# Performance work log

Hardware: AMD Instinct MI355X
Metric: run time of the kernel (lower is better)

The kernel has to match this reference:

```python
import jax, jax.numpy as jnp
import numpy as np
from jax import lax

H = 128  # hidden_size


def lstm_last_h(x, w_ih, w_hh, b_ih, b_hh):
    """PyTorch-style single-layer LSTM; returns final hidden state.
    x: (B, T, D). Gate order i, f, g, o. w_ih: (4H, D), w_hh: (4H, H)."""
    B = x.shape[0]
    Hh = w_hh.shape[1]
    x_proj = jnp.einsum('btd,gd->btg', x, w_ih) + b_ih + b_hh  # (B, T, 4H)

    def step(carry, xt):
        h, c = carry
        gates = xt + h @ w_hh.T
        i, f, g, o = jnp.split(gates, 4, axis=-1)
        i = jax.nn.sigmoid(i)
        f = jax.nn.sigmoid(f)
        g = jnp.tanh(g)
        o = jax.nn.sigmoid(o)
        c = f * c + i * g
        h = o * jnp.tanh(c)
        return (h, c), None

    init = (jnp.zeros((B, Hh), x.dtype), jnp.zeros((B, Hh), x.dtype))
    (h, _), _ = lax.scan(step, init, jnp.swapaxes(x_proj, 0, 1))
    return h  # (B, H)


def setup_inputs() -> dict:
    key = jax.random.key(0)
    ks = jax.random.split(key, 12)
    s = 0.05
    return {
        'x_players': jax.random.normal(ks[0], (64, 22, 128, 2), jnp.float32),
        'x_ball': jax.random.normal(ks[1], (64, 128, 2), jnp.float32),
        'p_w_ih': jax.random.normal(ks[2], (4 * H, 2), jnp.float32) * s,
        'p_w_hh': jax.random.normal(ks[3], (4 * H, H), jnp.float32) * s,
        'p_b_ih': jax.random.normal(ks[4], (4 * H,), jnp.float32) * s,
        'p_b_hh': jax.random.normal(ks[5], (4 * H,), jnp.float32) * s,
        'b_w_ih': jax.random.normal(ks[6], (4 * H, 2), jnp.float32) * s,
        'b_w_hh': jax.random.normal(ks[7], (4 * H, H), jnp.float32) * s,
        'b_b_ih': jax.random.normal(ks[8], (4 * H,), jnp.float32) * s,
        'b_b_hh': jax.random.normal(ks[9], (4 * H,), jnp.float32) * s,
        'fc_w': jax.random.normal(ks[10], (40, 2 * H), jnp.float32) * s,
        'fc_b': jax.random.normal(ks[11], (40,), jnp.float32) * s,
    }


def reference(x_players, x_ball, p_w_ih, p_w_hh, p_b_ih, p_b_hh,
              b_w_ih, b_w_hh, b_b_ih, b_b_hh, fc_w, fc_b):
    B, P, T, D = x_players.shape
    ball_h = lstm_last_h(x_ball, b_w_ih, b_w_hh, b_b_ih, b_b_hh)  # (B, H)
    # Shared player LSTM: fold players into batch (replaces per-player loop).
    ph = lstm_last_h(x_players.reshape(B * P, T, D),
                     p_w_ih, p_w_hh, p_b_ih, p_b_hh).reshape(B, P, H)
    ball_rep = jnp.broadcast_to(ball_h[:, None, :], (B, P, H))
    combined = jnp.concatenate([ph, ball_rep], axis=-1)  # (B, P, 2H)
    out = combined @ fc_w.T + fc_b  # (B, P, 40)
    return out.reshape(B, P, 20, 2)
```

## Files before the change

### kernel.cpp

```cpp
#include <hip/hip_runtime.h>


#define HDIM 128
#define TSTEPS 128
#define NPLAYER 1408
#define NSEQ 1472
#define NB 8
#define NBLK (NSEQ / NB)
#define NPBLK (NPLAYER / NB)
#define KT 5
#define BSTR 168
#define XSTR 258
#define HSTR 132

typedef _Float16 f16x8 __attribute__((ext_vector_type(8)));
typedef _Float16 f16x2 __attribute__((ext_vector_type(2)));
typedef float    f32x4 __attribute__((ext_vector_type(4)));
typedef float    f32x2 __attribute__((ext_vector_type(2)));

#define LOG2E 1.44269504f

__device__ __forceinline__ f32x2 exp2v(f32x2 a) {
    return (f32x2){__builtin_amdgcn_exp2f(a[0]), __builtin_amdgcn_exp2f(a[1])};
}
__device__ __forceinline__ f32x2 rcpv(f32x2 a) {
    return (f32x2){__builtin_amdgcn_rcpf(a[0]), __builtin_amdgcn_rcpf(a[1])};
}
__device__ __forceinline__ float dpp_sel8(float keep, float src) {
    return __int_as_float(__builtin_amdgcn_update_dpp(
        __float_as_int(keep), __float_as_int(src), 0x128 ,
        0xF, 0xC, false));
}

__global__ void __launch_bounds__(512)
__attribute__((amdgpu_waves_per_eu(2, 2)))
lstm_fc_kernel(const float* __restrict__ x_players, const float* __restrict__ x_ball,
               const float* __restrict__ p_w_ih, const float* __restrict__ p_w_hh,
               const float* __restrict__ p_b_ih, const float* __restrict__ p_b_hh,
               const float* __restrict__ b_w_ih, const float* __restrict__ b_w_hh,
               const float* __restrict__ b_b_ih, const float* __restrict__ b_b_hh,
               const float* __restrict__ fc_w, const float* __restrict__ fc_b,
               float* __restrict__ out)
{
    const int tid  = threadIdx.x;
    const int blk  = blockIdx.x;
    const int w    = tid >> 6;
    const int lane = tid & 63;
    const int nn   = lane & 15;
    const int q    = lane >> 4;

    const bool ball = (blk >= NPBLK);
    const float* w_ih = ball ? b_w_ih : p_w_ih;
    const float* w_hh = ball ? b_w_hh : p_w_hh;
    const float* bih  = ball ? b_b_ih : p_b_ih;
    const float* bhh  = ball ? b_b_hh : p_b_hh;
    const float* xg   = ball ? (x_ball    + (size_t)(blk - NPBLK) * NB * TSTEPS * 2)
                             : (x_players + (size_t)blk * NB * TSTEPS * 2);

    __shared__ __align__(16) _Float16 b_sh[2][NB * BSTR];
    __shared__ __align__(16) float x_sh[NB * XSTR];
    __shared__ __align__(16) float hbuf[NB * HSTR];
    __shared__ float vout[NB * 40];

    for (int i = tid; i < NB * 256; i += 512)
        x_sh[(i >> 8) * XSTR + (i & 255)] = xg[i];
    for (int i = tid; i < 2 * NB * BSTR / 2; i += 512)
        ((int*)b_sh)[i] = 0;

    f16x8 afr[4][KT];
    #pragma unroll
    for (int mi = 0; mi < 4; ++mi) {
        const int r = mi * HDIM + w * 16 + nn;
        const float* wr = w_hh + (size_t)r * HDIM;
        #pragma unroll
        for (int kt = 0; kt < 4; ++kt) {
            const float* p = wr + kt * 32 + q * 8;
            f16x8 a8;
            #pragma unroll
            for (int j = 0; j < 8; ++j) a8[j] = (_Float16)p[j];
            afr[mi][kt] = a8;
        }
        f16x8 a8 = {};
        if (q == 0) {
            a8[0] = (_Float16)w_ih[2 * r];
            a8[1] = (_Float16)w_ih[2 * r + 1];
            a8[2] = (_Float16)(bih[r] + bhh[r]);
        }
        afr[mi][4] = a8;
    }

    const int colh   = nn & 7;
    const int rowoff = (nn < 8) ? 0 : 2;
    const int hrow   = w * 16 + 4 * q + rowoff;
    f32x2 c = (f32x2){0.f, 0.f};
    f32x2 h = (f32x2){0.f, 0.f};

    f32x4 zero4 = (f32x4){0.f, 0.f, 0.f, 0.f};
    asm volatile("" : "+v"(zero4));

    __syncthreads();
    if (tid < NB) {
        _Float16* br0 = &b_sh[0][tid * BSTR];
        br0[128] = (_Float16)x_sh[tid * XSTR];
        br0[129] = (_Float16)x_sh[tid * XSTR + 1];
        br0[130] = (_Float16)1.0f;
        b_sh[1][tid * BSTR + 130] = (_Float16)1.0f;
    }
    __syncthreads();

    f16x8 bfr[KT] = {};

    auto substep = [&](int s, const _Float16* bc, _Float16* bn, bool last) {
        if (nn < 8) {
            #pragma unroll
            for (int kt = 0; kt < KT; ++kt)
                bfr[kt] = *(const f16x8*)(bc + nn * BSTR + kt * 32 + q * 8);
        }

        f32x4 acc[4];
        #pragma unroll
        for (int mi = 0; mi < 4; ++mi)
            acc[mi] = __builtin_amdgcn_mfma_f32_16x16x32_f16(afr[mi][4], bfr[4], zero4, 0, 0, 0);
        #pragma unroll
        for (int kt = 0; kt < 4; ++kt)
            #pragma unroll
            for (int mi = 0; mi < 4; ++mi)
                acc[mi] = __builtin_amdgcn_mfma_f32_16x16x32_f16(afr[mi][kt], bfr[kt], acc[mi], 0, 0, 0);

        if (!last && tid < NB) {
            const float x0 = x_sh[tid * XSTR + 2 * (s + 1)];
            const float x1 = x_sh[tid * XSTR + 2 * (s + 1) + 1];
            *(f16x2*)&bn[tid * BSTR + 128] = (f16x2){(_Float16)x0, (_Float16)x1};
        }

        f32x2 u[4];
        #pragma unroll
        for (int mi = 0; mi < 4; ++mi) {
            u[mi][0] = dpp_sel8(acc[mi][0], acc[mi][2]);
            u[mi][1] = dpp_sel8(acc[mi][1], acc[mi][3]);
        }

        const f32x2 ei = exp2v(u[0] * -LOG2E);
        const f32x2 ef = exp2v(u[1] * -LOG2E);
        const f32x2 eg = exp2v(u[2] * (2.0f * LOG2E));
        const f32x2 eo = exp2v(u[3] * -LOG2E);
        const f32x2 ig = (eg - 1.0f) * rcpv((ei + 1.0f) * (eg + 1.0f));
        const f32x2 ff = rcpv(ef + 1.0f);
        c = __builtin_elementwise_fma(ff, c, ig);
        c = __builtin_elementwise_min(__builtin_elementwise_max(c, (f32x2){-15.f, -15.f}),
                                      (f32x2){15.f, 15.f});
        const f32x2 ec = exp2v(c * (2.0f * LOG2E));
        h = (ec - 1.0f) * rcpv((eo + 1.0f) * (ec + 1.0f));

        if (!last) {
            *(f16x2*)&bn[colh * BSTR + hrow] = (f16x2){(_Float16)h[0], (_Float16)h[1]};
            __syncthreads();
        }
    };

    _Float16* b0 = &b_sh[0][0];
    _Float16* b1 = &b_sh[1][0];
    #pragma unroll 1
    for (int it = 0; it < TSTEPS / 2 - 1; ++it) {
        substep(2 * it,     b0, b1, false);
        substep(2 * it + 1, b1, b0, false);
        asm volatile("" : "+a"(afr[0][0]), "+a"(afr[0][1]), "+a"(afr[0][2]), "+a"(afr[0][3]), "+a"(afr[0][4]));
        asm volatile("" : "+a"(afr[1][0]), "+a"(afr[1][1]), "+a"(afr[1][2]), "+a"(afr[1][3]), "+a"(afr[1][4]));
        asm volatile("" : "+a"(afr[2][0]), "+a"(afr[2][1]), "+a"(afr[2][2]), "+a"(afr[2][3]), "+a"(afr[2][4]));
        asm volatile("" : "+a"(afr[3][0]), "+a"(afr[3][1]), "+a"(afr[3][2]), "+a"(afr[3][3]), "+a"(afr[3][4]));
        asm volatile("" : "+v"(zero4));
    }
    substep(126, b0, b1, false);
    substep(127, b1, b0, true);

    hbuf[colh * HSTR + hrow]     = h[0];
    hbuf[colh * HSTR + hrow + 1] = h[1];
    __syncthreads();

    if (!ball) {
        for (int o = tid; o < NB * 40; o += 512) {
            const int j = o / 40, row = o - j * 40;
            const float* wr = fc_w + (size_t)row * 2 * HDIM;
            const float* hp = &hbuf[j * HSTR];
            float a0 = fc_b[row], a1 = 0.f, a2 = 0.f, a3 = 0.f;
            #pragma unroll
            for (int k = 0; k < HDIM; k += 4) {
                float4 wv = *(const float4*)(wr + k);
                float4 hv = *(const float4*)(hp + k);
                a0 = __builtin_fmaf(wv.x, hv.x, a0);
                a1 = __builtin_fmaf(wv.y, hv.y, a1);
                a2 = __builtin_fmaf(wv.z, hv.z, a2);
                a3 = __builtin_fmaf(wv.w, hv.w, a3);
            }
            atomicAdd(&out[(size_t)(NB * blk + j) * 40 + row], (a0 + a1) + (a2 + a3));
        }
    } else {
        for (int o = tid; o < NB * 40; o += 512) {
            const int cc = o / 40, row = o - cc * 40;
            const float* wr = fc_w + (size_t)row * 2 * HDIM + HDIM;
            const float* hp = &hbuf[cc * HSTR];
            float a0 = 0.f, a1 = 0.f, a2 = 0.f, a3 = 0.f;
            #pragma unroll
            for (int k = 0; k < HDIM; k += 4) {
                float4 wv = *(const float4*)(wr + k);
                float4 hv = *(const float4*)(hp + k);
                a0 = __builtin_fmaf(wv.x, hv.x, a0);
                a1 = __builtin_fmaf(wv.y, hv.y, a1);
                a2 = __builtin_fmaf(wv.z, hv.z, a2);
                a3 = __builtin_fmaf(wv.w, hv.w, a3);
            }
            vout[cc * 40 + row] = (a0 + a1) + (a2 + a3);
        }
        __syncthreads();
        const int base_batch = (blk - NPBLK) * NB;
        for (int o = tid; o < NB * 22 * 40; o += 512) {
            const int cc = o / 880, rem = o - cc * 880;
            const int p = rem / 40, row = rem - p * 40;
            atomicAdd(&out[(size_t)((base_batch + cc) * 22 + p) * 40 + row],
                      vout[cc * 40 + row]);
        }
    }
}

extern "C" void kernel_launch(void* const* d_in, const int* in_sizes, int n_in,
                              void* d_out, int out_size, void* d_ws, size_t ws_size,
                              hipStream_t stream) {
    const float* x_players = (const float*)d_in[0];
    const float* x_ball    = (const float*)d_in[1];
    const float* p_w_ih    = (const float*)d_in[2];
    const float* p_w_hh    = (const float*)d_in[3];
    const float* p_b_ih    = (const float*)d_in[4];
    const float* p_b_hh    = (const float*)d_in[5];
    const float* b_w_ih    = (const float*)d_in[6];
    const float* b_w_hh    = (const float*)d_in[7];
    const float* b_b_ih    = (const float*)d_in[8];
    const float* b_b_hh    = (const float*)d_in[9];
    const float* fc_w      = (const float*)d_in[10];
    const float* fc_b      = (const float*)d_in[11];

    hipMemsetAsync(d_out, 0, (size_t)out_size * sizeof(float), stream);

    lstm_fc_kernel<<<dim3(NBLK), dim3(512), 0, stream>>>(
        x_players, x_ball, p_w_ih, p_w_hh, p_b_ih, p_b_hh,
        b_w_ih, b_w_hh, b_b_ih, b_b_hh, fc_w, fc_b, (float*)d_out);
}
```

Before: 181.8 us.

## Split gate work across 16 waves with flag-based producer/consumer exchange

Doubles the block to 1024 threads. Each wave now holds two gate tiles instead of four: waves 0-7 compute the i and g gates, and waves 8-15 compute the f and o gates. The f/o waves write their sigmoids to shared memory and raise a per-wave flag, while the i/g waves spin on that flag and then finish the cell and hidden-state update. This halves the serial MFMA and transcendental chain per wave and trades it for extra shared-memory traffic, spin-waits, a wider barrier and halved occupancy per block.

```diff
diff --git a/kernel.cpp b/kernel.cpp
--- a/kernel.cpp
+++ b/kernel.cpp
@@ -12,6 +12,7 @@
 #define BSTR 168
 #define XSTR 258
 #define HSTR 132
+#define ESTR 10
 
 typedef _Float16 f16x8 __attribute__((ext_vector_type(8)));
 typedef _Float16 f16x2 __attribute__((ext_vector_type(2)));
@@ -28,12 +29,11 @@
 }
 __device__ __forceinline__ float dpp_sel8(float keep, float src) {
     return __int_as_float(__builtin_amdgcn_update_dpp(
-        __float_as_int(keep), __float_as_int(src), 0x128 ,
-        0xF, 0xC, false));
-}
-
-__global__ void __launch_bounds__(512)
-__attribute__((amdgpu_waves_per_eu(2, 2)))
+        __float_as_int(keep), __float_as_int(src), 0x128 , 0xF, 0xC, false));
+}
+
+__global__ void __launch_bounds__(1024)
+__attribute__((amdgpu_waves_per_eu(4, 4)))
 lstm_fc_kernel(const float* __restrict__ x_players, const float* __restrict__ x_ball,
                const float* __restrict__ p_w_ih, const float* __restrict__ p_w_hh,
                const float* __restrict__ p_b_ih, const float* __restrict__ p_b_hh,
@@ -48,6 +48,9 @@
     const int lane = tid & 63;
     const int nn   = lane & 15;
     const int q    = lane >> 4;
+    const int b3   = (nn >> 3) & 1;
+    const int w8   = w & 7;
+    const bool heavy = (w < 8);
 
     const bool ball = (blk >= NPBLK);
     const float* w_ih = ball ? b_w_ih : p_w_ih;
@@ -59,18 +62,22 @@
 
     __shared__ __align__(16) _Float16 b_sh[2][NB * BSTR];
     __shared__ __align__(16) float x_sh[NB * XSTR];
+    __shared__ float exF[HDIM * ESTR];
+    __shared__ float exO[HDIM * ESTR];
+    __shared__ int   flags[8];
     __shared__ __align__(16) float hbuf[NB * HSTR];
     __shared__ float vout[NB * 40];
 
-    for (int i = tid; i < NB * 256; i += 512)
+    for (int i = tid; i < NB * 256; i += 1024)
         x_sh[(i >> 8) * XSTR + (i & 255)] = xg[i];
-    for (int i = tid; i < 2 * NB * BSTR / 2; i += 512)
+    for (int i = tid; i < 2 * NB * BSTR / 2; i += 1024)
         ((int*)b_sh)[i] = 0;
-
-    f16x8 afr[4][KT];
+    if (tid < 8) flags[tid] = 0;
+
+    f16x8 afr[2][KT];
     #pragma unroll
-    for (int mi = 0; mi < 4; ++mi) {
-        const int r = mi * HDIM + w * 16 + nn;
+    for (int ti = 0; ti < 2; ++ti) {
+        const int r = 16 * (w + 16 * ti) + nn;
         const float* wr = w_hh + (size_t)r * HDIM;
         #pragma unroll
         for (int kt = 0; kt < 4; ++kt) {
@@ -78,7 +85,7 @@
             f16x8 a8;
             #pragma unroll
             for (int j = 0; j < 8; ++j) a8[j] = (_Float16)p[j];
-            afr[mi][kt] = a8;
+            afr[ti][kt] = a8;
         }
         f16x8 a8 = {};
         if (q == 0) {
@@ -86,12 +93,11 @@
             a8[1] = (_Float16)w_ih[2 * r + 1];
             a8[2] = (_Float16)(bih[r] + bhh[r]);
         }
-        afr[mi][4] = a8;
-    }
-
-    const int colh   = nn & 7;
-    const int rowoff = (nn < 8) ? 0 : 2;
-    const int hrow   = w * 16 + 4 * q + rowoff;
+        afr[ti][4] = a8;
+    }
+
+    const int cc = nn & 7;
+    const int r0 = 16 * w8 + 4 * q + 2 * b3;
     f32x2 c = (f32x2){0.f, 0.f};
     f32x2 h = (f32x2){0.f, 0.f};
 
@@ -99,86 +105,96 @@
     asm volatile("" : "+v"(zero4));
 
     __syncthreads();
-    if (tid < NB) {
-        _Float16* br0 = &b_sh[0][tid * BSTR];
-        br0[128] = (_Float16)x_sh[tid * XSTR];
-        br0[129] = (_Float16)x_sh[tid * XSTR + 1];
+    if (tid >= 512 && tid < 512 + NB) {
+        const int j = tid - 512;
+        _Float16* br0 = &b_sh[0][j * BSTR];
+        br0[128] = (_Float16)x_sh[j * XSTR];
+        br0[129] = (_Float16)x_sh[j * XSTR + 1];
         br0[130] = (_Float16)1.0f;
-        b_sh[1][tid * BSTR + 130] = (_Float16)1.0f;
+        b_sh[1][j * BSTR + 130] = (_Float16)1.0f;
     }
     __syncthreads();
 
     f16x8 bfr[KT] = {};
 
-    auto substep = [&](int s, const _Float16* bc, _Float16* bn, bool last) {
+    #pragma unroll 1
+    for (int s = 0; s < TSTEPS; ++s) {
+        const bool last = (s == TSTEPS - 1);
+        const _Float16* bc = &b_sh[s & 1][0];
+        _Float16*       bn = &b_sh[(s & 1) ^ 1][0];
+
         if (nn < 8) {
             #pragma unroll
             for (int kt = 0; kt < KT; ++kt)
                 bfr[kt] = *(const f16x8*)(bc + nn * BSTR + kt * 32 + q * 8);
         }
 
-        f32x4 acc[4];
+        f32x4 acc[2];
         #pragma unroll
-        for (int mi = 0; mi < 4; ++mi)
-            acc[mi] = __builtin_amdgcn_mfma_f32_16x16x32_f16(afr[mi][4], bfr[4], zero4, 0, 0, 0);
+        for (int ti = 0; ti < 2; ++ti)
+            acc[ti] = __builtin_amdgcn_mfma_f32_16x16x32_f16(afr[ti][4], bfr[4], zero4, 0, 0, 0);
         #pragma unroll
         for (int kt = 0; kt < 4; ++kt)
             #pragma unroll
-            for (int mi = 0; mi < 4; ++mi)
-                acc[mi] = __builtin_amdgcn_mfma_f32_16x16x32_f16(afr[mi][kt], bfr[kt], acc[mi], 0, 0, 0);
-
-        if (!last && tid < NB) {
-            const float x0 = x_sh[tid * XSTR + 2 * (s + 1)];
-            const float x1 = x_sh[tid * XSTR + 2 * (s + 1) + 1];
-            *(f16x2*)&bn[tid * BSTR + 128] = (f16x2){(_Float16)x0, (_Float16)x1};
-        }
-
-        f32x2 u[4];
-        #pragma unroll
-        for (int mi = 0; mi < 4; ++mi) {
-            u[mi][0] = dpp_sel8(acc[mi][0], acc[mi][2]);
-            u[mi][1] = dpp_sel8(acc[mi][1], acc[mi][3]);
-        }
-
-        const f32x2 ei = exp2v(u[0] * -LOG2E);
-        const f32x2 ef = exp2v(u[1] * -LOG2E);
-        const f32x2 eg = exp2v(u[2] * (2.0f * LOG2E));
-        const f32x2 eo = exp2v(u[3] * -LOG2E);
-        const f32x2 ig = (eg - 1.0f) * rcpv((ei + 1.0f) * (eg + 1.0f));
-        const f32x2 ff = rcpv(ef + 1.0f);
-        c = __builtin_elementwise_fma(ff, c, ig);
-        c = __builtin_elementwise_min(__builtin_elementwise_max(c, (f32x2){-15.f, -15.f}),
-                                      (f32x2){15.f, 15.f});
-        const f32x2 ec = exp2v(c * (2.0f * LOG2E));
-        h = (ec - 1.0f) * rcpv((eo + 1.0f) * (ec + 1.0f));
-
-        if (!last) {
-            *(f16x2*)&bn[colh * BSTR + hrow] = (f16x2){(_Float16)h[0], (_Float16)h[1]};
-            __syncthreads();
-        }
-    };
-
-    _Float16* b0 = &b_sh[0][0];
-    _Float16* b1 = &b_sh[1][0];
-    #pragma unroll 1
-    for (int it = 0; it < TSTEPS / 2 - 1; ++it) {
-        substep(2 * it,     b0, b1, false);
-        substep(2 * it + 1, b1, b0, false);
+            for (int ti = 0; ti < 2; ++ti)
+                acc[ti] = __builtin_amdgcn_mfma_f32_16x16x32_f16(afr[ti][kt], bfr[kt], acc[ti], 0, 0, 0);
+
+        if (!last && tid >= 512 && tid < 512 + NB) {
+            const int j = tid - 512;
+            const float x0 = x_sh[j * XSTR + 2 * (s + 1)];
+            const float x1 = x_sh[j * XSTR + 2 * (s + 1) + 1];
+            *(f16x2*)&bn[j * BSTR + 128] = (f16x2){(_Float16)x0, (_Float16)x1};
+        }
+
+        f32x2 u0, u1;
+        u0[0] = dpp_sel8(acc[0][0], acc[0][2]);
+        u0[1] = dpp_sel8(acc[0][1], acc[0][3]);
+        u1[0] = dpp_sel8(acc[1][0], acc[1][2]);
+        u1[1] = dpp_sel8(acc[1][1], acc[1][3]);
+
+        if (!heavy) {
+            const f32x2 ef = exp2v(u0 * -LOG2E);
+            const f32x2 eo = exp2v(u1 * -LOG2E);
+            const f32x2 ff = rcpv(ef + 1.0f);
+            const f32x2 oo = rcpv(eo + 1.0f);
+            exF[r0 * ESTR + cc]       = ff[0];
+            exF[(r0 + 1) * ESTR + cc] = ff[1];
+            exO[r0 * ESTR + cc]       = oo[0];
+            exO[(r0 + 1) * ESTR + cc] = oo[1];
+            __threadfence_block();
+            if (lane == 0) ((volatile int*)flags)[w8] = s + 1;
+        } else {
+            const f32x2 ei = exp2v(u0 * -LOG2E);
+            const f32x2 eg = exp2v(u1 * (2.0f * LOG2E));
+            const f32x2 ig = (eg - 1.0f) * rcpv((ei + 1.0f) * (eg + 1.0f));
+            while (((volatile int*)flags)[w8] <= s) { }
+            __threadfence_block();
+            const f32x2 ff = (f32x2){exF[r0 * ESTR + cc], exF[(r0 + 1) * ESTR + cc]};
+            const f32x2 oo = (f32x2){exO[r0 * ESTR + cc], exO[(r0 + 1) * ESTR + cc]};
+            c = __builtin_elementwise_fma(ff, c, ig);
+            c = __builtin_elementwise_min(__builtin_elementwise_max(c, (f32x2){-15.f, -15.f}),
+                                          (f32x2){15.f, 15.f});
+            const f32x2 ec = exp2v(c * (2.0f * LOG2E));
+            h = oo * (ec - 1.0f) * rcpv(ec + 1.0f);
+            if (!last)
+                *(f16x2*)&bn[cc * BSTR + r0] = (f16x2){(_Float16)h[0], (_Float16)h[1]};
+        }
+
+        if (!last) __syncthreads();
+
         asm volatile("" : "+a"(afr[0][0]), "+a"(afr[0][1]), "+a"(afr[0][2]), "+a"(afr[0][3]), "+a"(afr[0][4]));
         asm volatile("" : "+a"(afr[1][0]), "+a"(afr[1][1]), "+a"(afr[1][2]), "+a"(afr[1][3]), "+a"(afr[1][4]));
-        asm volatile("" : "+a"(afr[2][0]), "+a"(afr[2][1]), "+a"(afr[2][2]), "+a"(afr[2][3]), "+a"(afr[2][4]));
-        asm volatile("" : "+a"(afr[3][0]), "+a"(afr[3][1]), "+a"(afr[3][2]), "+a"(afr[3][3]), "+a"(afr[3][4]));
         asm volatile("" : "+v"(zero4));
     }
-    substep(126, b0, b1, false);
-    substep(127, b1, b0, true);
-
-    hbuf[colh * HSTR + hrow]     = h[0];
-    hbuf[colh * HSTR + hrow + 1] = h[1];
+
+    if (heavy) {
+        hbuf[cc * HSTR + r0]     = h[0];
+        hbuf[cc * HSTR + r0 + 1] = h[1];
+    }
     __syncthreads();
 
     if (!ball) {
-        for (int o = tid; o < NB * 40; o += 512) {
+        for (int o = tid; o < NB * 40; o += 1024) {
             const int j = o / 40, row = o - j * 40;
             const float* wr = fc_w + (size_t)row * 2 * HDIM;
             const float* hp = &hbuf[j * HSTR];
@@ -195,10 +211,10 @@
             atomicAdd(&out[(size_t)(NB * blk + j) * 40 + row], (a0 + a1) + (a2 + a3));
         }
     } else {
-        for (int o = tid; o < NB * 40; o += 512) {
-            const int cc = o / 40, row = o - cc * 40;
+        for (int o = tid; o < NB * 40; o += 1024) {
+            const int cb = o / 40, row = o - cb * 40;
             const float* wr = fc_w + (size_t)row * 2 * HDIM + HDIM;
-            const float* hp = &hbuf[cc * HSTR];
+            const float* hp = &hbuf[cb * HSTR];
             float a0 = 0.f, a1 = 0.f, a2 = 0.f, a3 = 0.f;
             #pragma unroll
             for (int k = 0; k < HDIM; k += 4) {
@@ -209,15 +225,15 @@
                 a2 = __builtin_fmaf(wv.z, hv.z, a2);
                 a3 = __builtin_fmaf(wv.w, hv.w, a3);
             }
-            vout[cc * 40 + row] = (a0 + a1) + (a2 + a3);
+            vout[cb * 40 + row] = (a0 + a1) + (a2 + a3);
         }
         __syncthreads();
         const int base_batch = (blk - NPBLK) * NB;
-        for (int o = tid; o < NB * 22 * 40; o += 512) {
-            const int cc = o / 880, rem = o - cc * 880;
+        for (int o = tid; o < NB * 22 * 40; o += 1024) {
+            const int cb = o / 880, rem = o - cb * 880;
             const int p = rem / 40, row = rem - p * 40;
-            atomicAdd(&out[(size_t)((base_batch + cc) * 22 + p) * 40 + row],
-                      vout[cc * 40 + row]);
+            atomicAdd(&out[(size_t)((base_batch + cb) * 22 + p) * 40 + row],
+                      vout[cb * 40 + row]);
         }
     }
 }
@@ -240,7 +256,7 @@
 
     hipMemsetAsync(d_out, 0, (size_t)out_size * sizeof(float), stream);
 
-    lstm_fc_kernel<<<dim3(NBLK), dim3(512), 0, stream>>>(
+    lstm_fc_kernel<<<dim3(NBLK), dim3(1024), 0, stream>>>(
         x_players, x_ball, p_w_ih, p_w_hh, p_b_ih, p_b_hh,
         b_w_ih, b_w_hh, b_b_ih, b_b_hh, fc_w, fc_b, (float*)d_out);
 }
```

Measured after the change: 207.8 us. +14.3%, slower.
